# Kernel optimization log

Hardware: AMD Instinct MI355X
Metric: run time of the kernel (lower is better)

## Reference

```python
import jax, jax.numpy as jnp
import numpy as np

BATCH = 16384
IN = 1024
OUT = 1024
SIGMA_MIN = 0.1
SIGMA_MAX = 1.0


def setup_inputs() -> dict:
    key = jax.random.key(0)
    k0, k1, k2, k3 = jax.random.split(key, 4)
    x = jax.random.normal(k0, (BATCH, IN), dtype=jnp.float32)
    # torch init: triu(randn) -> upper-triangular reflector banks
    U = jnp.triu(jax.random.normal(k1, (IN, IN), dtype=jnp.float32))
    V = jnp.triu(jax.random.normal(k2, (OUT, OUT), dtype=jnp.float32))
    p = 0.001 * jax.random.normal(k3, (min(IN, OUT),), dtype=jnp.float32)
    bias = jnp.zeros((OUT,), dtype=jnp.float32)
    return {"x": x, "U": U, "V": V, "p": p, "bias": bias}


def _hprod_step(x, u):
    # u has zeros in its first i entries (triu row i), so the full-vector
    # form equals torch's sliced Hprod on the last k = n - i columns.
    alpha = 2.0 * (x @ u) / jnp.dot(u, u)          # [bs]
    return x - alpha[:, None] * u[None, :], None   # rank-1 update


def reference(x, U, V, p, bias):
    r = (SIGMA_MAX - SIGMA_MIN) / 2.0
    sigma_mean = SIGMA_MIN + r
    # mask enforces torch slice semantics (entries below diag never used)
    Um = U * jnp.triu(jnp.ones_like(U))
    Vm = V * jnp.triu(jnp.ones_like(V))
    # Umultiply: reflectors i = 0 .. n_U-1 in order (sequential recurrence)
    x, _ = jax.lax.scan(_hprod_step, x, Um)
    # Sigma: diagonal scaling (square case IN == OUT)
    sigmas = 2.0 * r * (jax.nn.sigmoid(p) - 0.5) + sigma_mean
    x = x * sigmas[None, :]
    # Vmultiply: reflectors i = n_V-1 .. 0 (reverse order)
    x, _ = jax.lax.scan(_hprod_step, x, Vm[::-1])
    return x + bias
```

## Files before the change

### kernel.cpp

```cpp
#include <hip/hip_runtime.h>
#include <stdint.h>

typedef __attribute__((ext_vector_type(8))) short short8;
typedef __attribute__((ext_vector_type(4))) float f32x4;

#define NN 1024
#define NBATCH 16384
#define ME ((size_t)NN * NN)
#define AS1 (const __attribute__((address_space(1))) void*)
#define AS3 (__attribute__((address_space(3))) void*)

__device__ __forceinline__ unsigned short f32_to_bf16_rne(float f) {
  unsigned int u = __float_as_uint(f);
  unsigned int r = (u + 0x7fffu + ((u >> 16) & 1u)) >> 16;
  return (unsigned short)r;
}

__device__ __forceinline__ unsigned int pack2bf(float lo, float hi) {
  return (unsigned int)f32_to_bf16_rne(lo) | ((unsigned int)f32_to_bf16_rne(hi) << 16);
}

__device__ __forceinline__ void split_bf16(float x, unsigned short& h, unsigned short& l) {
  h = f32_to_bf16_rne(x);
  float hf = __uint_as_float((unsigned int)h << 16);
  l = f32_to_bf16_rne(x - hf);
}

__device__ __forceinline__ float allsum64(float x) {
  x += __int_as_float(__builtin_amdgcn_update_dpp(0, __float_as_int(x), 0xB1, 0xF, 0xF, true));
  x += __int_as_float(__builtin_amdgcn_update_dpp(0, __float_as_int(x), 0x4E, 0xF, 0xF, true));
  x += __int_as_float(__builtin_amdgcn_update_dpp(0, __float_as_int(x), 0x141, 0xF, 0xF, true));
  x += __int_as_float(__builtin_amdgcn_update_dpp(0, __float_as_int(x), 0x140, 0xF, 0xF, true));
#if __has_builtin(__builtin_amdgcn_permlane16_swap) && __has_builtin(__builtin_amdgcn_permlane32_swap)
  {
    auto r16 = __builtin_amdgcn_permlane16_swap(__float_as_uint(x), __float_as_uint(x), false, false);
    x = __uint_as_float(r16[0]) + __uint_as_float(r16[1]);
    auto r32 = __builtin_amdgcn_permlane32_swap(__float_as_uint(x), __float_as_uint(x), false, false);
    x = __uint_as_float(r32[0]) + __uint_as_float(r32[1]);
  }
#else
  x += __int_as_float(__builtin_amdgcn_ds_swizzle(__float_as_int(x), 0x401F));
  x += __shfl_xor(x, 32);
#endif
  return x;
}

__global__ __launch_bounds__(256) void prep_kernel(
    const float* __restrict__ U, const float* __restrict__ V,
    const float* __restrict__ p, float* __restrict__ tau_u,
    float* __restrict__ tau_v, float* __restrict__ sigmas) {
  int wave = threadIdx.x >> 6, lane = threadIdx.x & 63;
  int row = blockIdx.x * 4 + wave;
  if (row < 2048) {
    const float* u = (row < NN) ? (U + (size_t)row * NN) : (V + (size_t)(row - NN) * NN);
    float s = 0.f;
#pragma unroll
    for (int t = 0; t < 16; ++t) { float a = u[lane + (t << 6)]; s += a * a; }
    s = allsum64(s);
    if (lane == 0) {
      float tau = 2.0f / s;
      if (row < NN) tau_u[row] = tau;
      else tau_v[row - NN] = tau;
    }
  } else if (row < 2064) {
    int j = ((row - 2048) << 6) + lane;
    float pj = p[j];
    float sg = 1.0f / (1.0f + expf(-pj));
    sigmas[j] = 0.9f * (sg - 0.5f) + 0.55f;
  }
}

__global__ __launch_bounds__(256) void castx_kernel(
    const float* __restrict__ X, unsigned short* __restrict__ Xb) {
  const size_t n4 = (size_t)NBATCH * NN / 4;
  for (size_t i = (size_t)blockIdx.x * 256 + threadIdx.x; i < n4; i += (size_t)gridDim.x * 256) {
    float4 v = reinterpret_cast<const float4*>(X)[i];
    uint2 o;
    o.x = pack2bf(v.x, v.y);
    o.y = pack2bf(v.z, v.w);
    reinterpret_cast<uint2*>(Xb)[i] = o;
  }
}

__global__ __launch_bounds__(64) void gram_t8_kernel(
    const float* __restrict__ U, const float* __restrict__ V,
    const float* __restrict__ tau_u, const float* __restrict__ tau_v,
    float* __restrict__ T8all) {
  __shared__ float G[64];
  const int blk = blockIdx.x;
  const int lane = threadIdx.x;
  const float* bank;
  int rbase, rsign, st;
  if (blk < 128) { bank = U; rbase = 8 * blk; rsign = 1; st = 8 * blk; }
  else { int s = blk - 128; bank = V; rbase = 1023 - 8 * s; rsign = -1; st = 1016 - 8 * s; }

  if (lane < 28) {
    int j = 1, k = 0, t = lane;
    for (int jj = 1; jj < 8; ++jj) {
      int lo = jj * (jj - 1) / 2, hi = jj * (jj + 1) / 2;
      if (t >= lo && t < hi) { j = jj; k = t - lo; }
    }
    const float* rk = bank + (size_t)(rbase + rsign * k) * NN;
    const float* rj = bank + (size_t)(rbase + rsign * j) * NN;
    float acc = 0.f;
    for (int i = st >> 2; i < 256; ++i) {
      float4 a = *reinterpret_cast<const float4*>(rk + 4 * i);
      float4 b = *reinterpret_cast<const float4*>(rj + 4 * i);
      acc += a.x * b.x + a.y * b.y + a.z * b.z + a.w * b.w;
    }
    G[k * 8 + j] = acc;
  }
  __syncthreads();

  if (lane < 8) {
    float Tr[8];
#pragma unroll
    for (int j = 0; j < 8; ++j) Tr[j] = 0.f;
#pragma unroll
    for (int j = 0; j < 8; ++j) {
      int grow = rbase + rsign * j;
      float tj = (blk < 128) ? tau_u[grow] : tau_v[grow];
      float a = 0.f;
#pragma unroll
      for (int k = 0; k < 8; ++k) {
        if (k < j) a += Tr[k] * G[k * 8 + j];
      }
      Tr[j] = (lane == j) ? tj : (-tj * a);
    }
#pragma unroll
    for (int j = 0; j < 8; ++j) T8all[(size_t)blk * 64 + lane * 8 + j] = Tr[j];
  }
}

__global__ __launch_bounds__(256) void splity_kernel(
    const float* __restrict__ U, const float* __restrict__ V,
    unsigned short* __restrict__ Yhi, unsigned short* __restrict__ Ylo,
    unsigned short* __restrict__ YThi, unsigned short* __restrict__ YTlo) {
  __shared__ float ys[128][129];
  const int tid = threadIdx.x;
  const int c = blockIdx.x >> 3, et = blockIdx.x & 7;
  const int half = tid & 1;
  const int slot = tid >> 1;
  const int e0 = et << 7;
  const int grow = (c < 8) ? ((c << 7) + slot) : (1023 - ((c - 8) << 7) - slot);
  const float* src = ((c < 8) ? U : V) + (size_t)grow * NN + e0 + (half << 6);
#pragma unroll
  for (int i = 0; i < 16; ++i) {
    float4 v4 = *reinterpret_cast<const float4*>(src + (i << 2));
    const int kk = (half << 6) + (i << 2);
    ys[slot][kk + 0] = v4.x; ys[slot][kk + 1] = v4.y;
    ys[slot][kk + 2] = v4.z; ys[slot][kk + 3] = v4.w;
  }
  __syncthreads();
  {
    const size_t rbase = ((size_t)(c * 128 + slot)) * NN + e0 + (half << 6);
#pragma unroll
    for (int i = 0; i < 16; ++i) {
      const int kk = (half << 6) + (i << 2);
      ushort4 h4, l4;
      split_bf16(ys[slot][kk + 0], h4.x, l4.x);
      split_bf16(ys[slot][kk + 1], h4.y, l4.y);
      split_bf16(ys[slot][kk + 2], h4.z, l4.z);
      split_bf16(ys[slot][kk + 3], h4.w, l4.w);
      *reinterpret_cast<ushort4*>(&Yhi[rbase + (i << 2)]) = h4;
      *reinterpret_cast<ushort4*>(&Ylo[rbase + (i << 2)]) = l4;
    }
  }
  {
    const int e = slot;
    const size_t tbase = ((size_t)c * 1024 + e0 + e) * 128 + (half << 6);
#pragma unroll
    for (int i = 0; i < 16; ++i) {
      const int k0 = (half << 6) + (i << 2);
      ushort4 h4, l4;
      split_bf16(ys[k0 + 0][e], h4.x, l4.x);
      split_bf16(ys[k0 + 1][e], h4.y, l4.y);
      split_bf16(ys[k0 + 2][e], h4.z, l4.z);
      split_bf16(ys[k0 + 3][e], h4.w, l4.w);
      *reinterpret_cast<ushort4*>(&YThi[tbase + (i << 2)]) = h4;
      *reinterpret_cast<ushort4*>(&YTlo[tbase + (i << 2)]) = l4;
    }
  }
}

#define LDK 40
#define BM 128
#define BN 128
#define BK 32

__global__ __launch_bounds__(256) void gramt_kernel(
    const unsigned short* __restrict__ Yhi, const unsigned short* __restrict__ Ylo,
    float* __restrict__ Gp) {
  __shared__ unsigned short Hs[128 * LDK];
  __shared__ unsigned short Ls[128 * LDK];
  const int tid = threadIdx.x;
  const int lane = tid & 63, wave = tid >> 6;
  const int c = blockIdx.x >> 3, ks = blockIdx.x & 7;
  const int wm = wave & 1, wn = wave >> 1;
  const int srow = tid >> 1, scol = (tid & 1) << 4;
  const unsigned short* ph = Yhi + ((size_t)(c * 128 + srow)) * NN + ks * 128 + scol;
  const unsigned short* pl = Ylo + ((size_t)(c * 128 + srow)) * NN + ks * 128 + scol;

  f32x4 acc[4][4];
#pragma unroll
  for (int a = 0; a < 4; ++a)
#pragma unroll
    for (int b = 0; b < 4; ++b) acc[a][b] = 0.f;

  const int arow0 = wm * 64, brow0 = wn * 64;
  const int fr = lane & 15, kb = (lane >> 4) << 3;

#pragma unroll 1
  for (int kt = 0; kt < 4; ++kt) {
    __syncthreads();
    *reinterpret_cast<uint4*>(&Hs[srow * LDK + scol]) = *reinterpret_cast<const uint4*>(ph + kt * 32);
    *reinterpret_cast<uint4*>(&Hs[srow * LDK + scol + 8]) = *reinterpret_cast<const uint4*>(ph + kt * 32 + 8);
    *reinterpret_cast<uint4*>(&Ls[srow * LDK + scol]) = *reinterpret_cast<const uint4*>(pl + kt * 32);
    *reinterpret_cast<uint4*>(&Ls[srow * LDK + scol + 8]) = *reinterpret_cast<const uint4*>(pl + kt * 32 + 8);
    __syncthreads();
    short8 ah[4], al[4], bh[4], bl[4];
#pragma unroll
    for (int tr = 0; tr < 4; ++tr) {
      ah[tr] = *reinterpret_cast<const short8*>(&Hs[(arow0 + tr * 16 + fr) * LDK + kb]);
      al[tr] = *reinterpret_cast<const short8*>(&Ls[(arow0 + tr * 16 + fr) * LDK + kb]);
    }
#pragma unroll
    for (int tc = 0; tc < 4; ++tc) {
      bh[tc] = *reinterpret_cast<const short8*>(&Hs[(brow0 + tc * 16 + fr) * LDK + kb]);
      bl[tc] = *reinterpret_cast<const short8*>(&Ls[(brow0 + tc * 16 + fr) * LDK + kb]);
    }
#pragma unroll
    for (int tr = 0; tr < 4; ++tr)
#pragma unroll
      for (int tc = 0; tc < 4; ++tc) {
        acc[tr][tc] = __builtin_amdgcn_mfma_f32_16x16x32_bf16(ah[tr], bh[tc], acc[tr][tc], 0, 0, 0);
        acc[tr][tc] = __builtin_amdgcn_mfma_f32_16x16x32_bf16(ah[tr], bl[tc], acc[tr][tc], 0, 0, 0);
        acc[tr][tc] = __builtin_amdgcn_mfma_f32_16x16x32_bf16(al[tr], bh[tc], acc[tr][tc], 0, 0, 0);
      }
  }
  const int rq = (lane >> 4) << 2;
#pragma unroll
  for (int tc = 0; tc < 4; ++tc) {
    const int gc = brow0 + tc * 16 + fr;
#pragma unroll
    for (int tr = 0; tr < 4; ++tr) {
      const int gr = arow0 + tr * 16 + rq;
#pragma unroll
      for (int q = 0; q < 4; ++q)
        Gp[(((size_t)c * 8 + ks) * 128 + gr + q) * 128 + gc] = acc[tr][tc][q];
    }
  }
}

__global__ __launch_bounds__(256) void gsum_tinit_kernel(
    const float* __restrict__ Gp, const float* __restrict__ T8all,
    float* __restrict__ G, float* __restrict__ Tg) {
  const int bid = blockIdx.x;
  if (bid < 1024) {
    const size_t i = (size_t)bid * 256 + threadIdx.x;
    const size_t c = i >> 14, rc = i & 16383;
    float s = 0.f;
#pragma unroll
    for (int sl = 0; sl < 8; ++sl)
      s += Gp[(c * 8 + sl) * 16384 + rc];
    G[i] = s;
  } else {
    const size_t base = ((size_t)(bid - 1024) * 256 + threadIdx.x) * 16;
#pragma unroll 1
    for (int e = 0; e < 16; ++e) {
      const size_t i = base + e;
      const int c = (int)(i >> 14), rc = (int)(i & 16383);
      const int r = rc >> 7, cl = rc & 127;
      float v = 0.f;
      if ((r >> 3) == (cl >> 3)) {
        const int sb = r >> 3;
        const int t8i = (c < 8) ? (16 * c + sb) : (128 + 16 * (c - 8) + sb);
        v = T8all[(size_t)t8i * 64 + (r & 7) * 8 + (cl & 7)];
      }
      Tg[i] = v;
    }
  }
}

template <int B>
__global__ __launch_bounds__(256) void tmerge_kernel(
    const float* __restrict__ G, float* __restrict__ Tg) {
  __shared__ float T1s[B * B], T2s[B * B], Gs[B * B], Xs[B * B];
  const int nm = 128 / (2 * B);
  const int c = blockIdx.x / nm, m = blockIdx.x % nm;
  const int a0 = 2 * B * m;
  const int tid = threadIdx.x;
  float* Tc = Tg + (size_t)c * 16384;
  for (int i = tid; i < B * B; i += 256) {
    const int r = i / B, cl = i % B;
    T1s[i] = Tc[(a0 + r) * 128 + a0 + cl];
    T2s[i] = Tc[(a0 + B + r) * 128 + a0 + B + cl];
    Gs[i] = G[((size_t)c * 128 + a0 + r) * 128 + a0 + B + cl];
  }
  __syncthreads();
  for (int i = tid; i < B * B; i += 256) {
    const int r = i / B, cl = i % B;
    float s = 0.f;
    for (int k = 0; k <= cl; ++k) s += Gs[r * B + k] * T2s[k * B + cl];
    Xs[i] = s;
  }
  __syncthreads();
  for (int i = tid; i < B * B; i += 256) {
    const int r = i / B, cl = i % B;
    float s = 0.f;
    for (int k = r; k < B; ++k) s -= T1s[r * B + k] * Xs[k * B + cl];
    Tc[(a0 + r) * 128 + a0 + B + cl] = s;
  }
}

__global__ __launch_bounds__(256) void tsplit_kernel(
    const float* __restrict__ Tg, unsigned short* __restrict__ Thi,
    unsigned short* __restrict__ Tlo) {
  const size_t i0 = ((size_t)blockIdx.x * 256 + threadIdx.x) * 16;
#pragma unroll
  for (int v = 0; v < 4; ++v) {
    float4 t = *reinterpret_cast<const float4*>(Tg + i0 + 4 * v);
    ushort4 h4, l4;
    split_bf16(t.x, h4.x, l4.x);
    split_bf16(t.y, h4.y, l4.y);
    split_bf16(t.z, h4.z, l4.z);
    split_bf16(t.w, h4.w, l4.w);
    *reinterpret_cast<ushort4*>(&Thi[i0 + 4 * v]) = h4;
    *reinterpret_cast<ushort4*>(&Tlo[i0 + 4 * v]) = l4;
  }
}

__global__ __launch_bounds__(256) void zw_kernel(
    const unsigned short* __restrict__ Thi, const unsigned short* __restrict__ Tlo,
    const unsigned short* __restrict__ YThi, const unsigned short* __restrict__ YTlo,
    unsigned short* __restrict__ WThi, unsigned short* __restrict__ WTlo) {
  __shared__ unsigned short Xh[128 * LDK], Xl[128 * LDK];
  __shared__ unsigned short Wh[128 * LDK], Wl[128 * LDK];
  const int tid = threadIdx.x;
  const int lane = tid & 63, wave = tid >> 6;
  const int c = blockIdx.x >> 3, bn = blockIdx.x & 7;
  const int n0 = bn * 128;
  const int wm = wave & 1, wn = wave >> 1;
  const int srow = tid >> 1, scol = (tid & 1) << 4;
  const unsigned short* pxh = Thi + ((size_t)c * 128 + srow) * 128 + scol;
  const unsigned short* pxl = Tlo + ((size_t)c * 128 + srow) * 128 + scol;
  const unsigned short* pwh = YThi + ((size_t)c * 1024 + n0 + srow) * 128 + scol;
  const unsigned short* pwl = YTlo + ((size_t)c * 1024 + n0 + srow) * 128 + scol;

  f32x4 acc[4][4];
#pragma unroll
  for (int a = 0; a < 4; ++a)
#pragma unroll
    for (int b = 0; b < 4; ++b) acc[a][b] = 0.f;

  const int arow0 = wm * 64, brow0 = wn * 64;
  const int fr = lane & 15, kb = (lane >> 4) << 3;

#pragma unroll 1
  for (int kt = 0; kt < 4; ++kt) {
    __syncthreads();
    *reinterpret_cast<uint4*>(&Xh[srow * LDK + scol]) = *reinterpret_cast<const uint4*>(pxh + kt * 32);
    *reinterpret_cast<uint4*>(&Xh[srow * LDK + scol + 8]) = *reinterpret_cast<const uint4*>(pxh + kt * 32 + 8);
    *reinterpret_cast<uint4*>(&Xl[srow * LDK + scol]) = *reinterpret_cast<const uint4*>(pxl + kt * 32);
    *reinterpret_cast<uint4*>(&Xl[srow * LDK + scol + 8]) = *reinterpret_cast<const uint4*>(pxl + kt * 32 + 8);
    *reinterpret_cast<uint4*>(&Wh[srow * LDK + scol]) = *reinterpret_cast<const uint4*>(pwh + kt * 32);
    *reinterpret_cast<uint4*>(&Wh[srow * LDK + scol + 8]) = *reinterpret_cast<const uint4*>(pwh + kt * 32 + 8);
    *reinterpret_cast<uint4*>(&Wl[srow * LDK + scol]) = *reinterpret_cast<const uint4*>(pwl + kt * 32);
    *reinterpret_cast<uint4*>(&Wl[srow * LDK + scol + 8]) = *reinterpret_cast<const uint4*>(pwl + kt * 32 + 8);
    __syncthreads();
    short8 ah[4], al[4], bh[4], bl[4];
#pragma unroll
    for (int tr = 0; tr < 4; ++tr) {
      ah[tr] = *reinterpret_cast<const short8*>(&Xh[(arow0 + tr * 16 + fr) * LDK + kb]);
      al[tr] = *reinterpret_cast<const short8*>(&Xl[(arow0 + tr * 16 + fr) * LDK + kb]);
    }
#pragma unroll
    for (int tc = 0; tc < 4; ++tc) {
      bh[tc] = *reinterpret_cast<const short8*>(&Wh[(brow0 + tc * 16 + fr) * LDK + kb]);
      bl[tc] = *reinterpret_cast<const short8*>(&Wl[(brow0 + tc * 16 + fr) * LDK + kb]);
    }
#pragma unroll
    for (int tr = 0; tr < 4; ++tr)
#pragma unroll
      for (int tc = 0; tc < 4; ++tc) {
        acc[tr][tc] = __builtin_amdgcn_mfma_f32_16x16x32_bf16(ah[tr], bh[tc], acc[tr][tc], 0, 0, 0);
        acc[tr][tc] = __builtin_amdgcn_mfma_f32_16x16x32_bf16(ah[tr], bl[tc], acc[tr][tc], 0, 0, 0);
        acc[tr][tc] = __builtin_amdgcn_mfma_f32_16x16x32_bf16(al[tr], bh[tc], acc[tr][tc], 0, 0, 0);
      }
  }
  const int rq = (lane >> 4) << 2;
#pragma unroll
  for (int tc = 0; tc < 4; ++tc) {
    const int gc = brow0 + tc * 16 + fr;
#pragma unroll
    for (int tr = 0; tr < 4; ++tr) {
      const int gr = arow0 + tr * 16 + rq;
      ushort4 h4, l4;
      split_bf16(acc[tr][tc][0], h4.x, l4.x);
      split_bf16(acc[tr][tc][1], h4.y, l4.y);
      split_bf16(acc[tr][tc][2], h4.z, l4.z);
      split_bf16(acc[tr][tc][3], h4.w, l4.w);
      const size_t off = ((size_t)c * 1024 + n0 + gc) * 128 + gr;
      *reinterpret_cast<ushort4*>(&WThi[off]) = h4;
      *reinterpret_cast<ushort4*>(&WTlo[off]) = l4;
    }
  }
}

__global__ __launch_bounds__(256) void chainc_kernel(
    const unsigned short* __restrict__ YThi, const unsigned short* __restrict__ YTlo,
    const unsigned short* __restrict__ WThi, const unsigned short* __restrict__ WTlo,
    unsigned short* __restrict__ chains) {
  __shared__ unsigned short Xh[128 * LDK], Xl[128 * LDK];
  __shared__ unsigned short Wh[128 * LDK], Wl[128 * LDK];
  const int tid = threadIdx.x;
  const int lane = tid & 63, wave = tid >> 6;
  const int c = blockIdx.x >> 6, b6 = blockIdx.x & 63;
  const int bm = b6 & 7, bn = b6 >> 3;
  const int m0 = bm * 128, n0 = bn * 128;
  const int wm = wave & 1, wn = wave >> 1;
  const int srow = tid >> 1, scol = (tid & 1) << 4;
  const unsigned short* pxh = YThi + ((size_t)c * 1024 + m0 + srow) * 128 + scol;
  const unsigned short* pxl = YTlo + ((size_t)c * 1024 + m0 + srow) * 128 + scol;
  const unsigned short* pwh = WThi + ((size_t)c * 1024 + n0 + srow) * 128 + scol;
  const unsigned short* pwl = WTlo + ((size_t)c * 1024 + n0 + srow) * 128 + scol;

  f32x4 acc[4][4];
#pragma unroll
  for (int a = 0; a < 4; ++a)
#pragma unroll
    for (int b = 0; b < 4; ++b) acc[a][b] = 0.f;

  const int arow0 = wm * 64, brow0 = wn * 64;
  const int fr = lane & 15, kb = (lane >> 4) << 3;

#pragma unroll 1
  for (int kt = 0; kt < 4; ++kt) {
    __syncthreads();
    *reinterpret_cast<uint4*>(&Xh[srow * LDK + scol]) = *reinterpret_cast<const uint4*>(pxh + kt * 32);
    *reinterpret_cast<uint4*>(&Xh[srow * LDK + scol + 8]) = *reinterpret_cast<const uint4*>(pxh + kt * 32 + 8);
    *reinterpret_cast<uint4*>(&Xl[srow * LDK + scol]) = *reinterpret_cast<const uint4*>(pxl + kt * 32);
    *reinterpret_cast<uint4*>(&Xl[srow * LDK + scol + 8]) = *reinterpret_cast<const uint4*>(pxl + kt * 32 + 8);
    *reinterpret_cast<uint4*>(&Wh[srow * LDK + scol]) = *reinterpret_cast<const uint4*>(pwh + kt * 32);
    *reinterpret_cast<uint4*>(&Wh[srow * LDK + scol + 8]) = *reinterpret_cast<const uint4*>(pwh + kt * 32 + 8);
    *reinterpret_cast<uint4*>(&Wl[srow * LDK + scol]) = *reinterpret_cast<const uint4*>(pwl + kt * 32);
    *reinterpret_cast<uint4*>(&Wl[srow * LDK + scol + 8]) = *reinterpret_cast<const uint4*>(pwl + kt * 32 + 8);
    __syncthreads();
    short8 ah[4], al[4], bh[4], bl[4];
#pragma unroll
    for (int tr = 0; tr < 4; ++tr) {
      ah[tr] = *reinterpret_cast<const short8*>(&Xh[(arow0 + tr * 16 + fr) * LDK + kb]);
      al[tr] = *reinterpret_cast<const short8*>(&Xl[(arow0 + tr * 16 + fr) * LDK + kb]);
    }
#pragma unroll
    for (int tc = 0; tc < 4; ++tc) {
      bh[tc] = *reinterpret_cast<const short8*>(&Wh[(brow0 + tc * 16 + fr) * LDK + kb]);
      bl[tc] = *reinterpret_cast<const short8*>(&Wl[(brow0 + tc * 16 + fr) * LDK + kb]);
    }
#pragma unroll
    for (int tr = 0; tr < 4; ++tr)
#pragma unroll
      for (int tc = 0; tc < 4; ++tc) {
        acc[tr][tc] = __builtin_amdgcn_mfma_f32_16x16x32_bf16(ah[tr], bh[tc], acc[tr][tc], 0, 0, 0);
        acc[tr][tc] = __builtin_amdgcn_mfma_f32_16x16x32_bf16(ah[tr], bl[tc], acc[tr][tc], 0, 0, 0);
        acc[tr][tc] = __builtin_amdgcn_mfma_f32_16x16x32_bf16(al[tr], bh[tc], acc[tr][tc], 0, 0, 0);
      }
  }
  unsigned short* dst = chains + (size_t)c * ME;
  const int rq = (lane >> 4) << 2;
  if ((c & 1) == 0) {
#pragma unroll
    for (int tc = 0; tc < 4; ++tc) {
      const int gcg = n0 + brow0 + tc * 16 + fr;
#pragma unroll
      for (int tr = 0; tr < 4; ++tr) {
        const int grg = m0 + arow0 + tr * 16 + rq;
#pragma unroll
        for (int q = 0; q < 4; ++q) {
          const float val = ((grg + q) == gcg ? 1.0f : 0.0f) - acc[tr][tc][q];
          dst[(size_t)(grg + q) * NN + gcg] = f32_to_bf16_rne(val);
        }
      }
    }
  } else {
#pragma unroll
    for (int tc = 0; tc < 4; ++tc) {
      const int gcg = n0 + brow0 + tc * 16 + fr;
#pragma unroll
      for (int tr = 0; tr < 4; ++tr) {
        const int grg = m0 + arow0 + tr * 16 + rq;
        ushort4 pk;
        pk.x = f32_to_bf16_rne(((grg + 0) == gcg ? 1.0f : 0.0f) - acc[tr][tc][0]);
        pk.y = f32_to_bf16_rne(((grg + 1) == gcg ? 1.0f : 0.0f) - acc[tr][tc][1]);
        pk.z = f32_to_bf16_rne(((grg + 2) == gcg ? 1.0f : 0.0f) - acc[tr][tc][2]);
        pk.w = f32_to_bf16_rne(((grg + 3) == gcg ? 1.0f : 0.0f) - acc[tr][tc][3]);
        *reinterpret_cast<ushort4*>(&dst[(size_t)gcg * NN + grg]) = pk;
      }
    }
  }
}

__device__ __forceinline__ void cb_stage(
    const unsigned short* __restrict__ agbase, const unsigned short* __restrict__ bgbase,
    unsigned short* __restrict__ la, unsigned short* __restrict__ lb, int tid, int kt) {
#pragma unroll
  for (int i = 0; i < 2; ++i) {
    const int slot = tid + 256 * i;
    const int row = slot >> 2, s = slot & 3;
    __builtin_amdgcn_global_load_lds(
        AS1(agbase + (size_t)row * NN + kt * 32 + s * 8), AS3(la + row * 32 + s * 8), 16, 0, 0);
  }
#pragma unroll
  for (int i = 0; i < 2; ++i) {
    const int slot = tid + 256 * i;
    const int row = slot >> 2, s = slot & 3;
    __builtin_amdgcn_global_load_lds(
        AS1(bgbase + (size_t)row * NN + kt * 32 + s * 8), AS3(lb + row * 32 + s * 8), 16, 0, 0);
  }
}

__device__ __forceinline__ void cb_compute(
    const unsigned short* __restrict__ As, const unsigned short* __restrict__ Bs,
    f32x4 acc[4][4], int arow0, int brow0, int fr, int kb) {
  short8 af[4], bf[4];
#pragma unroll
  for (int tr = 0; tr < 4; ++tr)
    af[tr] = *reinterpret_cast<const short8*>(&As[(arow0 + tr * 16 + fr) * 32 + kb]);
#pragma unroll
  for (int tc = 0; tc < 4; ++tc)
    bf[tc] = *reinterpret_cast<const short8*>(&Bs[(brow0 + tc * 16 + fr) * 32 + kb]);
#pragma unroll
  for (int tr = 0; tr < 4; ++tr)
#pragma unroll
    for (int tc = 0; tc < 4; ++tc)
      acc[tr][tc] = __builtin_amdgcn_mfma_f32_16x16x32_bf16(af[tr], bf[tc], acc[tr][tc], 0, 0, 0);
}

__device__ __forceinline__ void compose_body(
    const unsigned short* __restrict__ Xb, const unsigned short* __restrict__ Wb,
    unsigned short* __restrict__ Op, const float* __restrict__ sig, int b, bool tstore) {
  __shared__ unsigned short As[3][BM * 32];
  __shared__ unsigned short Bs[3][BN * 32];
  const int tid = threadIdx.x;
  const int lane = tid & 63, wave = tid >> 6;
  const int bm = b & 7, bn = b >> 3;
  const int m0 = bm * BM, n0 = bn * BN;
  const int wm = wave & 1, wn = wave >> 1;
  const int arow0 = wm * 64, brow0 = wn * 64;
  const int fr = lane & 15, kb = (lane >> 4) << 3;

  f32x4 acc[4][4];
#pragma unroll
  for (int a = 0; a < 4; ++a)
#pragma unroll
    for (int bb = 0; bb < 4; ++bb) acc[a][bb] = 0.f;

  const unsigned short* agbase = Xb + (size_t)m0 * NN;
  const unsigned short* bgbase = Wb + (size_t)n0 * NN;

  cb_stage(agbase, bgbase, &As[0][0], &Bs[0][0], tid, 0);
  cb_stage(agbase, bgbase, &As[1][0], &Bs[1][0], tid, 1);
#pragma unroll 1
  for (int kt = 0; kt < 31; ++kt) {
    asm volatile("s_waitcnt vmcnt(4)" ::: "memory");
    __builtin_amdgcn_s_barrier();
    __builtin_amdgcn_sched_barrier(0);
    if (kt + 2 < 32) {
      const int nb = (kt + 2) % 3;
      cb_stage(agbase, bgbase, &As[nb][0], &Bs[nb][0], tid, kt + 2);
    }
    cb_compute(&As[kt % 3][0], &Bs[kt % 3][0], acc, arow0, brow0, fr, kb);
  }
  asm volatile("s_waitcnt vmcnt(0)" ::: "memory");
  __builtin_amdgcn_s_barrier();
  __builtin_amdgcn_sched_barrier(0);
  cb_compute(&As[1][0], &Bs[1][0], acc, arow0, brow0, fr, kb);

  const int rq = (lane >> 4) << 2;
  if (!tstore) {
#pragma unroll
    for (int tc = 0; tc < 4; ++tc) {
      const int gc = n0 + brow0 + tc * 16 + fr;
      const float s = sig ? sig[gc] : 1.0f;
#pragma unroll
      for (int tr = 0; tr < 4; ++tr) {
        const int gr = m0 + arow0 + tr * 16 + rq;
#pragma unroll
        for (int q = 0; q < 4; ++q) {
          Op[(size_t)(gr + q) * NN + gc] = f32_to_bf16_rne(acc[tr][tc][q] * s);
        }
      }
    }
  } else {
#pragma unroll
    for (int tc = 0; tc < 4; ++tc) {
      const int gc = n0 + brow0 + tc * 16 + fr;
#pragma unroll
      for (int tr = 0; tr < 4; ++tr) {
        const int gr = m0 + arow0 + tr * 16 + rq;
        ushort4 pk;
        pk.x = f32_to_bf16_rne(acc[tr][tc][0]);
        pk.y = f32_to_bf16_rne(acc[tr][tc][1]);
        pk.z = f32_to_bf16_rne(acc[tr][tc][2]);
        pk.w = f32_to_bf16_rne(acc[tr][tc][3]);
        *reinterpret_cast<ushort4*>(&Op[(size_t)gc * NN + gr]) = pk;
      }
    }
  }
}

__global__ __launch_bounds__(256) void composeL1_kernel(
    const unsigned short* __restrict__ ch, unsigned short* __restrict__ P) {
  const int sub = blockIdx.x >> 6, b = blockIdx.x & 63;
  const int i = sub & 3;
  const unsigned short* x = ch + (size_t)((sub < 4 ? 0 : 8) + 2 * i) * ME;
  compose_body(x, x + ME, P + (size_t)sub * ME, nullptr, b, (i & 1) != 0);
}

__global__ __launch_bounds__(256) void composeL2_kernel(
    const unsigned short* __restrict__ P, unsigned short* __restrict__ Q) {
  const int sub = blockIdx.x >> 6, b = blockIdx.x & 63;
  compose_body(P + (size_t)(2 * sub) * ME, P + (size_t)(2 * sub + 1) * ME,
               Q + (size_t)sub * ME, nullptr, b, (sub & 1) != 0);
}

__global__ __launch_bounds__(256) void composeL3_kernel(
    const unsigned short* __restrict__ Q, const float* __restrict__ sigmas,
    unsigned short* __restrict__ F) {
  const int sub = blockIdx.x >> 6, b = blockIdx.x & 63;
  if (sub == 0) compose_body(Q, Q + ME, F, sigmas, b, false);
  else compose_body(Q + 2 * ME, Q + 3 * ME, F + ME, nullptr, b, true);
}

__global__ __launch_bounds__(256) void composeL4_kernel(
    const unsigned short* __restrict__ F, unsigned short* __restrict__ Mt) {
  compose_body(F + ME, F, Mt, nullptr, blockIdx.x, false);
}

__global__ __launch_bounds__(512) void gemm256_kernel(
    const unsigned short* __restrict__ Xb, const unsigned short* __restrict__ Mt,
    const float* __restrict__ bias, float* __restrict__ Out) {
  __shared__ unsigned short As[3][256 * 32];
  __shared__ unsigned short Bs[3][128 * 32];
  const int tid = threadIdx.x;
  const int lane = tid & 63, wave = tid >> 6;
  const int bm = blockIdx.x & 63, bn = blockIdx.x >> 6;
  const int m0 = bm * 256, n0 = bn * 128;
  const int wm = wave & 3, wn = wave >> 2;
  const int arow0 = wm * 64, brow0 = wn * 64;
  const int fr = lane & 15, kb = (lane >> 4) << 3;

  f32x4 acc[4][4];
#pragma unroll
  for (int a = 0; a < 4; ++a)
#pragma unroll
    for (int b = 0; b < 4; ++b) acc[a][b] = 0.f;

  const unsigned short* agbase = Xb + (size_t)m0 * NN;
  const unsigned short* bgbase = Mt + (size_t)n0 * NN;

#define G256_STAGE(B, KT)                                                        \
  {                                                                              \
    _Pragma("unroll")                                                            \
    for (int i = 0; i < 2; ++i) {                                                \
      const int slot = tid + 512 * i;                                            \
      const int row = slot >> 2, s = slot & 3;                                   \
      __builtin_amdgcn_global_load_lds(                                          \
          AS1(agbase + (size_t)row * NN + (KT) * 32 + s * 8),                    \
          AS3(&As[B][row * 32 + s * 8]), 16, 0, 0);                              \
    }                                                                            \
    {                                                                            \
      const int row = tid >> 2, s = tid & 3;                                     \
      __builtin_amdgcn_global_load_lds(                                          \
          AS1(bgbase + (size_t)row * NN + (KT) * 32 + s * 8),                    \
          AS3(&Bs[B][row * 32 + s * 8]), 16, 0, 0);                              \
    }                                                                            \
  }

#define G256_CMP(B)                                                              \
  {                                                                              \
    short8 af[4], bf4[4];                                                        \
    _Pragma("unroll")                                                            \
    for (int tr = 0; tr < 4; ++tr)                                               \
      af[tr] = *reinterpret_cast<const short8*>(&As[B][(arow0 + tr * 16 + fr) * 32 + kb]); \
    _Pragma("unroll")                                                            \
    for (int tc = 0; tc < 4; ++tc)                                               \
      bf4[tc] = *reinterpret_cast<const short8*>(&Bs[B][(brow0 + tc * 16 + fr) * 32 + kb]); \
    _Pragma("unroll")                                                            \
    for (int tr = 0; tr < 4; ++tr)                                               \
      _Pragma("unroll")                                                          \
      for (int tc = 0; tc < 4; ++tc)                                             \
        acc[tr][tc] = __builtin_amdgcn_mfma_f32_16x16x32_bf16(af[tr], bf4[tc], acc[tr][tc], 0, 0, 0); \
  }

  G256_STAGE(0, 0)
  G256_STAGE(1, 1)
#pragma unroll 1
  for (int kt = 0; kt < 31; ++kt) {
    asm volatile("s_waitcnt vmcnt(3)" ::: "memory");
    __builtin_amdgcn_s_barrier();
    __builtin_amdgcn_sched_barrier(0);
    if (kt + 2 < 32) {
      const int nb = (kt + 2) % 3;
      G256_STAGE(nb, kt + 2)
    }
    G256_CMP(kt % 3)
  }
  asm volatile("s_waitcnt vmcnt(0)" ::: "memory");
  __builtin_amdgcn_s_barrier();
  __builtin_amdgcn_sched_barrier(0);
  G256_CMP(1)
#undef G256_STAGE
#undef G256_CMP

  const int rq = (lane >> 4) << 2;
#pragma unroll
  for (int tc = 0; tc < 4; ++tc) {
    const int gc = n0 + brow0 + tc * 16 + fr;
    const float bv = bias[gc];
#pragma unroll
    for (int tr = 0; tr < 4; ++tr) {
      const int gr = m0 + arow0 + tr * 16 + rq;
#pragma unroll
      for (int q = 0; q < 4; ++q) {
        Out[(size_t)(gr + q) * NN + gc] = acc[tr][tc][q] + bv;
      }
    }
  }
}

__global__ __launch_bounds__(256) void gemm_fb_kernel(
    const float* __restrict__ X, const unsigned short* __restrict__ Mt,
    const float* __restrict__ bias, float* __restrict__ Out) {
  __shared__ float Af[2][BM * 32];
  __shared__ unsigned short Bsl[2][BN * 32];
  const int tid = threadIdx.x;
  const int lane = tid & 63, wave = tid >> 6;
  const int bm = blockIdx.x & 127;
  const int bn = blockIdx.x >> 7;
  const int m0 = bm * BM, n0 = bn * BN;
  const int wm = wave & 1, wn = wave >> 1;
  const int arow0 = wm * 64, brow0 = wn * 64;
  const int fr = lane & 15, kb = (lane >> 4) << 3;

  f32x4 acc[4][4];
#pragma unroll
  for (int a = 0; a < 4; ++a)
#pragma unroll
    for (int b = 0; b < 4; ++b) acc[a][b] = 0.f;

  const float* agbase = X + (size_t)m0 * NN;
  const unsigned short* bgbase = Mt + (size_t)n0 * NN;

#define FB_STAGE(PB, KT)                                                        \
  {                                                                             \
    _Pragma("unroll")                                                           \
    for (int i = 0; i < 4; ++i) {                                               \
      const int slot = tid + 256 * i;                                           \
      const int row = slot >> 3, s = slot & 7;                                  \
      __builtin_amdgcn_global_load_lds(                                         \
          AS1(agbase + (size_t)row * NN + (KT) * 32 + s * 4),                   \
          AS3(&Af[PB][row * 32 + s * 4]), 16, 0, 0);                            \
    }                                                                           \
    _Pragma("unroll")                                                           \
    for (int i = 0; i < 2; ++i) {                                               \
      const int slot = tid + 256 * i;                                           \
      const int row = slot >> 2, s = slot & 3;                                  \
      __builtin_amdgcn_global_load_lds(                                         \
          AS1(bgbase + (size_t)row * NN + (KT) * 32 + s * 8),                   \
          AS3(&Bsl[PB][row * 32 + s * 8]), 16, 0, 0);                           \
    }                                                                           \
  }

  FB_STAGE(0, 0)
  int pb = 0;
#pragma unroll 1
  for (int kt = 0; kt < 32; ++kt) {
    __syncthreads();
    if (kt + 1 < 32) FB_STAGE(pb ^ 1, kt + 1)
    {
      short8 af[4], bf[4];
      const int c0 = kb >> 2;
#pragma unroll
      for (int tr = 0; tr < 4; ++tr) {
        const int row = arow0 + tr * 16 + fr;
        const f32x4 a0 = *reinterpret_cast<const f32x4*>(&Af[pb][row * 32 + c0 * 4]);
        const f32x4 a1 = *reinterpret_cast<const f32x4*>(&Af[pb][row * 32 + (c0 + 1) * 4]);
        uint4 w;
        w.x = pack2bf(a0[0], a0[1]); w.y = pack2bf(a0[2], a0[3]);
        w.z = pack2bf(a1[0], a1[1]); w.w = pack2bf(a1[2], a1[3]);
        af[tr] = *reinterpret_cast<const short8*>(&w);
      }
#pragma unroll
      for (int tc = 0; tc < 4; ++tc) {
        const int row = brow0 + tc * 16 + fr;
        bf[tc] = *reinterpret_cast<const short8*>(&Bsl[pb][row * 32 + kb]);
      }
#pragma unroll
      for (int tr = 0; tr < 4; ++tr)
#pragma unroll
        for (int tc = 0; tc < 4; ++tc)
          acc[tr][tc] = __builtin_amdgcn_mfma_f32_16x16x32_bf16(af[tr], bf[tc], acc[tr][tc], 0, 0, 0);
    }
    pb ^= 1;
  }
#undef FB_STAGE

  const int rq = (lane >> 4) << 2;
#pragma unroll
  for (int tc = 0; tc < 4; ++tc) {
    const int gc = n0 + brow0 + tc * 16 + fr;
    const float bv = bias[gc];
#pragma unroll
    for (int tr = 0; tr < 4; ++tr) {
      const int gr = m0 + arow0 + tr * 16 + rq;
#pragma unroll
      for (int q = 0; q < 4; ++q) {
        Out[(size_t)(gr + q) * NN + gc] = acc[tr][tc][q] + bv;
      }
    }
  }
}

extern "C" void kernel_launch(void* const* d_in, const int* in_sizes, int n_in,
                              void* d_out, int out_size, void* d_ws, size_t ws_size,
                              hipStream_t stream) {
  const float* x = (const float*)d_in[0];
  const float* U = (const float*)d_in[1];
  const float* V = (const float*)d_in[2];
  const float* p = (const float*)d_in[3];
  const float* bias = (const float*)d_in[4];
  float* out = (float*)d_out;

  char* ws = (char*)d_ws;
  float* tau_u = (float*)(ws);
  float* tau_v = (float*)(ws + 4096);
  float* sigmas = (float*)(ws + 8192);
  float* T8all = (float*)(ws + 16384);
  unsigned short* Mt = (unsigned short*)(ws + 81920);

  const size_t XB_OFF = 4u * 1024 * 1024;
  const size_t XB_BYTES = (size_t)NBATCH * NN * 2;
  const bool fast = ws_size >= XB_OFF + XB_BYTES;
  unsigned short* Xb = (unsigned short*)(ws + XB_OFF);

  unsigned short* sc = (unsigned short*)d_out;
  unsigned short* chains = sc;
  unsigned short* P = sc + 16 * ME;
  unsigned short* Q = sc + 24 * ME;
  unsigned short* F = sc + 28 * ME;
  unsigned short* YThi = sc + 16 * ME;
  unsigned short* YTlo = sc + 18 * ME;
  unsigned short* WThi = sc + 20 * ME;
  unsigned short* WTlo = sc + 22 * ME;
  unsigned short* Yhi = sc + 24 * ME;
  unsigned short* Ylo = sc + 26 * ME;
  float* Gp = (float*)(sc + 28 * ME);
  float* G = (float*)sc;
  float* Tg = (float*)(sc + ME);
  unsigned short* Thi = sc + 24 * ME;
  unsigned short* Tlo = Thi + 262144;

  prep_kernel<<<516, 256, 0, stream>>>(U, V, p, tau_u, tau_v, sigmas);
  if (fast) castx_kernel<<<2048, 256, 0, stream>>>(x, Xb);
  gram_t8_kernel<<<256, 64, 0, stream>>>(U, V, tau_u, tau_v, T8all);
  splity_kernel<<<128, 256, 0, stream>>>(U, V, Yhi, Ylo, YThi, YTlo);
  gramt_kernel<<<128, 256, 0, stream>>>(Yhi, Ylo, Gp);
  gsum_tinit_kernel<<<1088, 256, 0, stream>>>(Gp, T8all, G, Tg);
  tmerge_kernel<8><<<128, 256, 0, stream>>>(G, Tg);
  tmerge_kernel<16><<<64, 256, 0, stream>>>(G, Tg);
  tmerge_kernel<32><<<32, 256, 0, stream>>>(G, Tg);
  tmerge_kernel<64><<<16, 256, 0, stream>>>(G, Tg);
  tsplit_kernel<<<64, 256, 0, stream>>>(Tg, Thi, Tlo);
  zw_kernel<<<128, 256, 0, stream>>>(Thi, Tlo, YThi, YTlo, WThi, WTlo);
  chainc_kernel<<<1024, 256, 0, stream>>>(YThi, YTlo, WThi, WTlo, chains);
  composeL1_kernel<<<512, 256, 0, stream>>>(chains, P);
  composeL2_kernel<<<256, 256, 0, stream>>>(P, Q);
  composeL3_kernel<<<128, 256, 0, stream>>>(Q, sigmas, F);
  composeL4_kernel<<<64, 256, 0, stream>>>(F, Mt);
  if (fast) gemm256_kernel<<<512, 512, 0, stream>>>(Xb, Mt, bias, out);
  else gemm_fb_kernel<<<1024, 256, 0, stream>>>(x, Mt, bias, out);
}
```

Baseline: 325.2 us.

## Skip structurally-zero blocks in chain composition and XOR-swizzle LDS tiles

Uses the upper-triangular structure of the reflector banks to find output tiles of the Gram, chain and compose stages that are identity or zero. Those tiles are written directly instead of being computed through MFMA loops. Separately, the global-to-LDS loads and fragment reads in the compose and main GEMM kernels get an XOR swizzle on the 8-element column chunk to reduce LDS bank conflicts. The risk is correctness if the zero-block bounds (z0) per chain level are wrong.

```diff
diff --git a/kernel.cpp b/kernel.cpp
--- a/kernel.cpp
+++ b/kernel.cpp
@@ -191,11 +191,18 @@
 __global__ __launch_bounds__(256) void gramt_kernel(
     const unsigned short* __restrict__ Yhi, const unsigned short* __restrict__ Ylo,
     float* __restrict__ Gp) {
+  const int tid = threadIdx.x;
+  const int c = blockIdx.x >> 3, ks = blockIdx.x & 7;
+  const bool productive = (c < 8) ? (ks >= c) : (ks >= 7 - (c - 8));
+  if (!productive) {
+    float4 z = {0.f, 0.f, 0.f, 0.f};
+    float4* dst = reinterpret_cast<float4*>(Gp + (((size_t)c * 8 + ks) << 14));
+    for (int i = tid; i < 4096; i += 256) dst[i] = z;
+    return;
+  }
   __shared__ unsigned short Hs[128 * LDK];
   __shared__ unsigned short Ls[128 * LDK];
-  const int tid = threadIdx.x;
   const int lane = tid & 63, wave = tid >> 6;
-  const int c = blockIdx.x >> 3, ks = blockIdx.x & 7;
   const int wm = wave & 1, wn = wave >> 1;
   const int srow = tid >> 1, scol = (tid & 1) << 4;
   const unsigned short* ph = Yhi + ((size_t)(c * 128 + srow)) * NN + ks * 128 + scol;
@@ -411,14 +418,52 @@
     const unsigned short* __restrict__ YThi, const unsigned short* __restrict__ YTlo,
     const unsigned short* __restrict__ WThi, const unsigned short* __restrict__ WTlo,
     unsigned short* __restrict__ chains) {
-  __shared__ unsigned short Xh[128 * LDK], Xl[128 * LDK];
-  __shared__ unsigned short Wh[128 * LDK], Wl[128 * LDK];
   const int tid = threadIdx.x;
   const int lane = tid & 63, wave = tid >> 6;
   const int c = blockIdx.x >> 6, b6 = blockIdx.x & 63;
   const int bm = b6 & 7, bn = b6 >> 3;
   const int m0 = bm * 128, n0 = bn * 128;
   const int wm = wave & 1, wn = wave >> 1;
+  const int arow0 = wm * 64, brow0 = wn * 64;
+  const int fr = lane & 15, kb = (lane >> 4) << 3;
+  const int rq = (lane >> 4) << 2;
+  unsigned short* dst = chains + (size_t)c * ME;
+
+  const int z0 = (c < 8) ? (128 * c) : (896 - 128 * (c - 8));
+  if (m0 < z0 || n0 < z0) {
+    if ((c & 1) == 0) {
+#pragma unroll
+      for (int tc = 0; tc < 4; ++tc) {
+        const int gcg = n0 + brow0 + tc * 16 + fr;
+#pragma unroll
+        for (int tr = 0; tr < 4; ++tr) {
+          const int grg = m0 + arow0 + tr * 16 + rq;
+#pragma unroll
+          for (int q = 0; q < 4; ++q)
+            dst[(size_t)(grg + q) * NN + gcg] = f32_to_bf16_rne((grg + q) == gcg ? 1.0f : 0.0f);
+        }
+      }
+    } else {
+#pragma unroll
+      for (int tc = 0; tc < 4; ++tc) {
+        const int gcg = n0 + brow0 + tc * 16 + fr;
+#pragma unroll
+        for (int tr = 0; tr < 4; ++tr) {
+          const int grg = m0 + arow0 + tr * 16 + rq;
+          ushort4 pk;
+          pk.x = f32_to_bf16_rne((grg + 0) == gcg ? 1.0f : 0.0f);
+          pk.y = f32_to_bf16_rne((grg + 1) == gcg ? 1.0f : 0.0f);
+          pk.z = f32_to_bf16_rne((grg + 2) == gcg ? 1.0f : 0.0f);
+          pk.w = f32_to_bf16_rne((grg + 3) == gcg ? 1.0f : 0.0f);
+          *reinterpret_cast<ushort4*>(&dst[(size_t)gcg * NN + grg]) = pk;
+        }
+      }
+    }
+    return;
+  }
+
+  __shared__ unsigned short Xh[128 * LDK], Xl[128 * LDK];
+  __shared__ unsigned short Wh[128 * LDK], Wl[128 * LDK];
   const int srow = tid >> 1, scol = (tid & 1) << 4;
   const unsigned short* pxh = YThi + ((size_t)c * 1024 + m0 + srow) * 128 + scol;
   const unsigned short* pxl = YTlo + ((size_t)c * 1024 + m0 + srow) * 128 + scol;
@@ -430,9 +475,6 @@
   for (int a = 0; a < 4; ++a)
 #pragma unroll
     for (int b = 0; b < 4; ++b) acc[a][b] = 0.f;
-
-  const int arow0 = wm * 64, brow0 = wn * 64;
-  const int fr = lane & 15, kb = (lane >> 4) << 3;
 
 #pragma unroll 1
   for (int kt = 0; kt < 4; ++kt) {
@@ -466,8 +508,6 @@
         acc[tr][tc] = __builtin_amdgcn_mfma_f32_16x16x32_bf16(al[tr], bh[tc], acc[tr][tc], 0, 0, 0);
       }
   }
-  unsigned short* dst = chains + (size_t)c * ME;
-  const int rq = (lane >> 4) << 2;
   if ((c & 1) == 0) {
 #pragma unroll
     for (int tc = 0; tc < 4; ++tc) {
@@ -507,15 +547,17 @@
   for (int i = 0; i < 2; ++i) {
     const int slot = tid + 256 * i;
     const int row = slot >> 2, s = slot & 3;
+    const int cs = s ^ ((row >> 1) & 3);
     __builtin_amdgcn_global_load_lds(
-        AS1(agbase + (size_t)row * NN + kt * 32 + s * 8), AS3(la + row * 32 + s * 8), 16, 0, 0);
+        AS1(agbase + (size_t)row * NN + kt * 32 + cs * 8), AS3(la + row * 32 + s * 8), 16, 0, 0);
   }
 #pragma unroll
   for (int i = 0; i < 2; ++i) {
     const int slot = tid + 256 * i;
     const int row = slot >> 2, s = slot & 3;
+    const int cs = s ^ ((row >> 1) & 3);
     __builtin_amdgcn_global_load_lds(
-        AS1(bgbase + (size_t)row * NN + kt * 32 + s * 8), AS3(lb + row * 32 + s * 8), 16, 0, 0);
+        AS1(bgbase + (size_t)row * NN + kt * 32 + cs * 8), AS3(lb + row * 32 + s * 8), 16, 0, 0);
   }
 }
 
@@ -523,12 +565,19 @@
     const unsigned short* __restrict__ As, const unsigned short* __restrict__ Bs,
     f32x4 acc[4][4], int arow0, int brow0, int fr, int kb) {
   short8 af[4], bf[4];
-#pragma unroll
-  for (int tr = 0; tr < 4; ++tr)
-    af[tr] = *reinterpret_cast<const short8*>(&As[(arow0 + tr * 16 + fr) * 32 + kb]);
-#pragma unroll
-  for (int tc = 0; tc < 4; ++tc)
-    bf[tc] = *reinterpret_cast<const short8*>(&Bs[(brow0 + tc * 16 + fr) * 32 + kb]);
+  const int ck = kb >> 3;
+#pragma unroll
+  for (int tr = 0; tr < 4; ++tr) {
+    const int row = arow0 + tr * 16 + fr;
+    const int sl = ck ^ ((row >> 1) & 3);
+    af[tr] = *reinterpret_cast<const short8*>(&As[row * 32 + sl * 8]);
+  }
+#pragma unroll
+  for (int tc = 0; tc < 4; ++tc) {
+    const int row = brow0 + tc * 16 + fr;
+    const int sl = ck ^ ((row >> 1) & 3);
+    bf[tc] = *reinterpret_cast<const short8*>(&Bs[row * 32 + sl * 8]);
+  }
 #pragma unroll
   for (int tr = 0; tr < 4; ++tr)
 #pragma unroll
@@ -538,9 +587,8 @@
 
 __device__ __forceinline__ void compose_body(
     const unsigned short* __restrict__ Xb, const unsigned short* __restrict__ Wb,
-    unsigned short* __restrict__ Op, const float* __restrict__ sig, int b, bool tstore) {
-  __shared__ unsigned short As[3][BM * 32];
-  __shared__ unsigned short Bs[3][BN * 32];
+    unsigned short* __restrict__ Op, const float* __restrict__ sig, int b, bool tstore,
+    int z0) {
   const int tid = threadIdx.x;
   const int lane = tid & 63, wave = tid >> 6;
   const int bm = b & 7, bn = b >> 3;
@@ -548,7 +596,43 @@
   const int wm = wave & 1, wn = wave >> 1;
   const int arow0 = wm * 64, brow0 = wn * 64;
   const int fr = lane & 15, kb = (lane >> 4) << 3;
-
+  const int rq = (lane >> 4) << 2;
+
+  if (m0 < z0 || n0 < z0) {
+    if (!tstore) {
+#pragma unroll
+      for (int tc = 0; tc < 4; ++tc) {
+        const int gc = n0 + brow0 + tc * 16 + fr;
+        const float s = sig ? sig[gc] : 1.0f;
+#pragma unroll
+        for (int tr = 0; tr < 4; ++tr) {
+          const int gr = m0 + arow0 + tr * 16 + rq;
+#pragma unroll
+          for (int q = 0; q < 4; ++q)
+            Op[(size_t)(gr + q) * NN + gc] = f32_to_bf16_rne((gr + q == gc) ? s : 0.0f);
+        }
+      }
+    } else {
+#pragma unroll
+      for (int tc = 0; tc < 4; ++tc) {
+        const int gc = n0 + brow0 + tc * 16 + fr;
+#pragma unroll
+        for (int tr = 0; tr < 4; ++tr) {
+          const int gr = m0 + arow0 + tr * 16 + rq;
+          ushort4 pk;
+          pk.x = f32_to_bf16_rne((gr + 0 == gc) ? 1.0f : 0.0f);
+          pk.y = f32_to_bf16_rne((gr + 1 == gc) ? 1.0f : 0.0f);
+          pk.z = f32_to_bf16_rne((gr + 2 == gc) ? 1.0f : 0.0f);
+          pk.w = f32_to_bf16_rne((gr + 3 == gc) ? 1.0f : 0.0f);
+          *reinterpret_cast<ushort4*>(&Op[(size_t)gc * NN + gr]) = pk;
+        }
+      }
+    }
+    return;
+  }
+
+  __shared__ unsigned short As[3][BM * 32];
+  __shared__ unsigned short Bs[3][BN * 32];
   f32x4 acc[4][4];
 #pragma unroll
   for (int a = 0; a < 4; ++a)
@@ -576,7 +660,6 @@
   __builtin_amdgcn_sched_barrier(0);
   cb_compute(&As[1][0], &Bs[1][0], acc, arow0, brow0, fr, kb);
 
-  const int rq = (lane >> 4) << 2;
   if (!tstore) {
 #pragma unroll
     for (int tc = 0; tc < 4; ++tc) {
@@ -614,27 +697,29 @@
   const int sub = blockIdx.x >> 6, b = blockIdx.x & 63;
   const int i = sub & 3;
   const unsigned short* x = ch + (size_t)((sub < 4 ? 0 : 8) + 2 * i) * ME;
-  compose_body(x, x + ME, P + (size_t)sub * ME, nullptr, b, (i & 1) != 0);
+  const int z0 = (sub < 4) ? (256 * i) : (768 - 256 * i);
+  compose_body(x, x + ME, P + (size_t)sub * ME, nullptr, b, (i & 1) != 0, z0);
 }
 
 __global__ __launch_bounds__(256) void composeL2_kernel(
     const unsigned short* __restrict__ P, unsigned short* __restrict__ Q) {
   const int sub = blockIdx.x >> 6, b = blockIdx.x & 63;
+  const int z0 = (sub == 1 || sub == 2) ? 512 : 0;
   compose_body(P + (size_t)(2 * sub) * ME, P + (size_t)(2 * sub + 1) * ME,
-               Q + (size_t)sub * ME, nullptr, b, (sub & 1) != 0);
+               Q + (size_t)sub * ME, nullptr, b, (sub & 1) != 0, z0);
 }
 
 __global__ __launch_bounds__(256) void composeL3_kernel(
     const unsigned short* __restrict__ Q, const float* __restrict__ sigmas,
     unsigned short* __restrict__ F) {
   const int sub = blockIdx.x >> 6, b = blockIdx.x & 63;
-  if (sub == 0) compose_body(Q, Q + ME, F, sigmas, b, false);
-  else compose_body(Q + 2 * ME, Q + 3 * ME, F + ME, nullptr, b, true);
+  if (sub == 0) compose_body(Q, Q + ME, F, sigmas, b, false, 0);
+  else compose_body(Q + 2 * ME, Q + 3 * ME, F + ME, nullptr, b, true, 0);
 }
 
 __global__ __launch_bounds__(256) void composeL4_kernel(
     const unsigned short* __restrict__ F, unsigned short* __restrict__ Mt) {
-  compose_body(F + ME, F, Mt, nullptr, blockIdx.x, false);
+  compose_body(F + ME, F, Mt, nullptr, blockIdx.x, false, 0);
 }
 
 __global__ __launch_bounds__(512) void gemm256_kernel(
@@ -665,14 +750,16 @@
     for (int i = 0; i < 2; ++i) {                                                \
       const int slot = tid + 512 * i;                                            \
       const int row = slot >> 2, s = slot & 3;                                   \
+      const int cs = s ^ ((row >> 1) & 3);                                       \
       __builtin_amdgcn_global_load_lds(                                          \
-          AS1(agbase + (size_t)row * NN + (KT) * 32 + s * 8),                    \
+          AS1(agbase + (size_t)row * NN + (KT) * 32 + cs * 8),                   \
           AS3(&As[B][row * 32 + s * 8]), 16, 0, 0);                              \
     }                                                                            \
     {                                                                            \
       const int row = tid >> 2, s = tid & 3;                                     \
+      const int cs = s ^ ((row >> 1) & 3);                                       \
       __builtin_amdgcn_global_load_lds(                                          \
-          AS1(bgbase + (size_t)row * NN + (KT) * 32 + s * 8),                    \
+          AS1(bgbase + (size_t)row * NN + (KT) * 32 + cs * 8),                   \
           AS3(&Bs[B][row * 32 + s * 8]), 16, 0, 0);                              \
     }                                                                            \
   }
@@ -680,12 +767,19 @@
 #define G256_CMP(B)                                                              \
   {                                                                              \
     short8 af[4], bf4[4];                                                        \
+    const int ck = kb >> 3;                                                      \
     _Pragma("unroll")                                                            \
-    for (int tr = 0; tr < 4; ++tr)                                               \
-      af[tr] = *reinterpret_cast<const short8*>(&As[B][(arow0 + tr * 16 + fr) * 32 + kb]); \
+    for (int tr = 0; tr < 4; ++tr) {                                             \
+      const int row = arow0 + tr * 16 + fr;                                      \
+      const int sl = ck ^ ((row >> 1) & 3);                                      \
+      af[tr] = *reinterpret_cast<const short8*>(&As[B][row * 32 + sl * 8]);      \
+    }                                                                            \
     _Pragma("unroll")                                                            \
-    for (int tc = 0; tc < 4; ++tc)                                               \
-      bf4[tc] = *reinterpret_cast<const short8*>(&Bs[B][(brow0 + tc * 16 + fr) * 32 + kb]); \
+    for (int tc = 0; tc < 4; ++tc) {                                             \
+      const int row = brow0 + tc * 16 + fr;                                      \
+      const int sl = ck ^ ((row >> 1) & 3);                                      \
+      bf4[tc] = *reinterpret_cast<const short8*>(&Bs[B][row * 32 + sl * 8]);     \
+    }                                                                            \
     _Pragma("unroll")                                                            \
     for (int tr = 0; tr < 4; ++tr)                                               \
       _Pragma("unroll")                                                          \
```

Measured after the change: 318.1 us. -2.2%, faster.
